# Kernel optimization log

Hardware: AMD Instinct MI355X
Metric: run time of the kernel (lower is better)

Reference implementation:

```python
import jax, jax.numpy as jnp
import numpy as np

N_NODES = 100000
N_EDGES = 1250000
D_FEAT = 64


def setup_inputs() -> dict:
    key = jax.random.key(0)
    kx, ke = jax.random.split(key)
    x = jax.random.normal(kx, (N_NODES, D_FEAT), dtype=jnp.float32)
    edge_index = jax.random.randint(ke, (2, N_EDGES), 0, N_NODES, dtype=jnp.int64)
    return {"x": x, "edge_index": edge_index}


def _aggregate(x, src, dst, num_nodes):
    # out[i] = sum_{e: dst[e]==i} x[src[e]]  (identity message, 'add' aggr)
    return jax.ops.segment_sum(x[src], dst, num_segments=num_nodes)


def reference(x, edge_index):
    num_nodes = x.shape[0]
    src, dst = edge_index[0], edge_index[1]  # PyG source_to_target flow
    h = _aggregate(x, src, dst, num_nodes)   # conv1
    h = jax.nn.relu(h)
    h = _aggregate(h, src, dst, num_nodes)   # conv2
    return h
```

## Files before the change

### kernel.cpp

```cpp
#include <hip/hip_runtime.h>
#include <hip/hip_bf16.h>


#define N_FEAT    64
#define BIN_SHIFT 7
#define BIN_NODES 128
#define CAPBIN    2048
#define NB_H      784
#define NSCAN     1024
#define GSTRIDE   16
#define TILE      4096
#define PTHREADS  512
#define EPT       8
#define NPTR      (BIN_NODES + 1)
#define SRCSH     14

typedef unsigned int u32;
typedef unsigned short u16;
typedef __attribute__((ext_vector_type(8))) unsigned short u16x8;
typedef __attribute__((ext_vector_type(4))) unsigned int u32x4;
typedef __attribute__((ext_vector_type(2))) float f32x2;

__device__ inline u16 f2bf(float f) {
    u32 u = __builtin_bit_cast(u32, f);
    return (u16)((u + 0x7FFFu + ((u >> 16) & 1u)) >> 16);
}

__global__ __launch_bounds__(256) void convert_kernel(
    const float* __restrict__ xf, u16* __restrict__ xb, int n_elems)
{
    int i = ((int)blockIdx.x * 256 + (int)threadIdx.x) * 8;
    if (i < n_elems) {
        float4 a = *(const float4*)(xf + i);
        float4 b = *(const float4*)(xf + i + 4);
        u16x8 r;
        r[0]=f2bf(a.x); r[1]=f2bf(a.y); r[2]=f2bf(a.z); r[3]=f2bf(a.w);
        r[4]=f2bf(b.x); r[5]=f2bf(b.y); r[6]=f2bf(b.z); r[7]=f2bf(b.w);
        *(u16x8*)(xb + i) = r;
    }
}

__global__ __launch_bounds__(PTHREADS) void partition_kernel(
    const int* __restrict__ src, const int* __restrict__ dst,
    u32* __restrict__ gcur,
    u32* __restrict__ cbdata,
    int n_edges, int n_bins)
{
    __shared__ u32 hist[NSCAN];
    __shared__ u32 starts[NSCAN];
    __shared__ u32 lpos[NSCAN];
    __shared__ u32 wcur[NB_H];
    __shared__ u32 sortbuf[TILE];
    __shared__ u16 binid[TILE];
    __shared__ u32 wsum[PTHREADS / 64];

    const int tid   = threadIdx.x;
    const int tbase = (int)blockIdx.x * TILE;
    const int tend  = min(tbase + TILE, n_edges);

    for (int i = tid; i < NSCAN; i += PTHREADS) { hist[i] = 0; lpos[i] = 0; }
    __syncthreads();

    u32 breg[EPT];
    u32 preg[EPT];
    #pragma unroll
    for (int k = 0; k < EPT; ++k) {
        int e = tbase + tid + k * PTHREADS;
        breg[k] = ~0u;
        if (e < tend) {
            int d = dst[e];
            int s = src[e];
            breg[k] = (u32)d >> BIN_SHIFT;
            preg[k] = ((u32)(d & (BIN_NODES - 1)) << 17) | (u32)s;
            atomicAdd(&hist[breg[k]], 1u);
        }
    }
    __syncthreads();

    {
        const int b0 = tid * 2;
        u32 h0 = hist[b0], h1 = hist[b0 + 1];
        u32 s  = h0 + h1;
        u32 inc = s;
        #pragma unroll
        for (int d = 1; d < 64; d <<= 1) {
            u32 o = __shfl_up(inc, d);
            if ((tid & 63) >= d) inc += o;
        }
        if ((tid & 63) == 63) wsum[tid >> 6] = inc;
        __syncthreads();
        u32 woff = 0;
        #pragma unroll
        for (int k = 0; k < PTHREADS / 64; ++k) if (k < (tid >> 6)) woff += wsum[k];
        u32 excl = woff + inc - s;
        starts[b0]     = excl;
        starts[b0 + 1] = excl + h0;
    }
    __syncthreads();

    const int rot = (int)(((u32)blockIdx.x * 193u) % (u32)n_bins);
    for (int i = tid; i < n_bins; i += PTHREADS) {
        int b = i + rot; if (b >= n_bins) b -= n_bins;
        u32 h = hist[b];
        if (h) wcur[b] = atomicAdd(&gcur[b * GSTRIDE], h);
    }
    __syncthreads();

    #pragma unroll
    for (int k = 0; k < EPT; ++k) {
        if (breg[k] != ~0u) {
            u32 b   = breg[k];
            u32 pos = starts[b] + atomicAdd(&lpos[b], 1u);
            sortbuf[pos] = preg[k];
            binid[pos]   = (u16)b;
        }
    }
    __syncthreads();

    const int cnt = tend - tbase;
    for (int j = tid; j < cnt; j += PTHREADS) {
        u32 b   = binid[j];
        u32 rel = wcur[b] + ((u32)j - starts[b]);
        if (rel < CAPBIN)
            cbdata[(size_t)b * CAPBIN + rel] = sortbuf[j];
    }
}

__global__ __launch_bounds__(256) void sort_aggregate_kernel(
    const u16* __restrict__ xin,
    u32* __restrict__ cbdata,
    const u32* __restrict__ gcur,
    u32* __restrict__ nodeptr,
    u16* __restrict__ out_bf,
    int n_nodes, int n_bins)
{
    __shared__ u32 hist[NSCAN];
    __shared__ u32 starts[NSCAN];
    __shared__ u32 lpos[NSCAN];
    __shared__ u32 sl[CAPBIN];
    __shared__ u32 wsum[4];

    const int tid = threadIdx.x;
    const int bin = blockIdx.x;
    if (bin >= n_bins) return;

    for (int i = tid; i < NSCAN; i += 256) { hist[i] = 0; lpos[i] = 0; }
    __syncthreads();

    int cnt = (int)gcur[bin * GSTRIDE];
    if (cnt > CAPBIN) cnt = CAPBIN;
    u32* bd = cbdata + (size_t)bin * CAPBIN;

    for (int j = tid; j < cnt; j += 256) {
        u32 p = bd[j];
        u32 key = ((p >> 17) << 3) | ((p & 0x1FFFFu) >> SRCSH);
        atomicAdd(&hist[key], 1u);
    }
    __syncthreads();

    {
        const int b0 = tid * 4;
        u32 h0 = hist[b0], h1 = hist[b0+1], h2 = hist[b0+2], h3 = hist[b0+3];
        u32 s  = h0 + h1 + h2 + h3;
        u32 inc = s;
        #pragma unroll
        for (int d = 1; d < 64; d <<= 1) {
            u32 o = __shfl_up(inc, d);
            if ((tid & 63) >= d) inc += o;
        }
        if ((tid & 63) == 63) wsum[tid >> 6] = inc;
        __syncthreads();
        u32 woff = 0;
        #pragma unroll
        for (int k = 0; k < 4; ++k) if (k < (tid >> 6)) woff += wsum[k];
        u32 excl = woff + inc - s;
        starts[b0]   = excl;
        starts[b0+1] = excl + h0;
        starts[b0+2] = excl + h0 + h1;
        starts[b0+3] = excl + h0 + h1 + h2;
    }
    __syncthreads();

    for (int j = tid; j < cnt; j += 256) {
        u32 p   = bd[j];
        u32 key = ((p >> 17) << 3) | ((p & 0x1FFFFu) >> SRCSH);
        u32 pos = starts[key] + atomicAdd(&lpos[key], 1u);
        sl[pos] = p & 0x1FFFFu;
    }
    __syncthreads();

    const u32 base = (u32)bin * CAPBIN;
    for (int j = tid; j < cnt; j += 256)
        bd[j] = sl[j];
    if (tid < BIN_NODES)
        nodeptr[(size_t)bin * NPTR + tid] = base + starts[tid << 3];
    if (tid == 0)
        nodeptr[(size_t)bin * NPTR + BIN_NODES] = base + (u32)cnt;

    const int w    = tid >> 6;
    const int lane = tid & 63;
    const int grp  = lane >> 3;
    const int sub  = lane & 7;
    const char* xc = (const char*)xin;

    #pragma unroll 1
    for (int rep = 0; rep < 4; ++rep) {
        const int nid  = w * 8 + grp + rep * 32;
        const int node = bin * BIN_NODES + nid;
        const int s0 = (int)starts[nid << 3];
        const int s1 = (nid < BIN_NODES - 1) ? (int)starts[(nid + 1) << 3] : cnt;

        f32x2 a0={0.f,0.f}, a1={0.f,0.f}, a2={0.f,0.f}, a3={0.f,0.f};

        int jb = s0;
        for (; jb + 8 <= s1; jb += 8) {
            #pragma unroll
            for (int k = 0; k < 8; ++k) {
                u32 s = sl[jb + k];
                u32x4 v = *(const u32x4*)(xc + ((size_t)s << 7) + (sub << 4));
                a0 += (f32x2){ __builtin_bit_cast(float, v[0] << 16),
                               __builtin_bit_cast(float, v[0] & 0xFFFF0000u) };
                a1 += (f32x2){ __builtin_bit_cast(float, v[1] << 16),
                               __builtin_bit_cast(float, v[1] & 0xFFFF0000u) };
                a2 += (f32x2){ __builtin_bit_cast(float, v[2] << 16),
                               __builtin_bit_cast(float, v[2] & 0xFFFF0000u) };
                a3 += (f32x2){ __builtin_bit_cast(float, v[3] << 16),
                               __builtin_bit_cast(float, v[3] & 0xFFFF0000u) };
            }
        }
        #pragma unroll 1
        for (; jb < s1; ++jb) {
            u32 s = sl[jb];
            u32x4 v = *(const u32x4*)(xc + ((size_t)s << 7) + (sub << 4));
            a0 += (f32x2){ __builtin_bit_cast(float, v[0] << 16),
                           __builtin_bit_cast(float, v[0] & 0xFFFF0000u) };
            a1 += (f32x2){ __builtin_bit_cast(float, v[1] << 16),
                           __builtin_bit_cast(float, v[1] & 0xFFFF0000u) };
            a2 += (f32x2){ __builtin_bit_cast(float, v[2] << 16),
                           __builtin_bit_cast(float, v[2] & 0xFFFF0000u) };
            a3 += (f32x2){ __builtin_bit_cast(float, v[3] << 16),
                           __builtin_bit_cast(float, v[3] & 0xFFFF0000u) };
        }

        if (node < n_nodes) {
            u16x8 o;
            o[0]=f2bf(fmaxf(a0.x,0.f)); o[1]=f2bf(fmaxf(a0.y,0.f));
            o[2]=f2bf(fmaxf(a1.x,0.f)); o[3]=f2bf(fmaxf(a1.y,0.f));
            o[4]=f2bf(fmaxf(a2.x,0.f)); o[5]=f2bf(fmaxf(a2.y,0.f));
            o[6]=f2bf(fmaxf(a3.x,0.f)); o[7]=f2bf(fmaxf(a3.y,0.f));
            *(u16x8*)(out_bf + (size_t)node * N_FEAT + sub * 8) = o;
        }
    }
}

__global__ __launch_bounds__(256) void aggregate_kernel(
    const u16* __restrict__ xin,
    const u32* __restrict__ csorted,
    const u32* __restrict__ nodeptr,
    float* __restrict__ out_f,
    int n_nodes)
{
    const int tid  = threadIdx.x;

    const int w    = tid >> 6;
    const int lane = tid & 63;
    const int grp  = lane >> 3;
    const int sub  = lane & 7;
    const char* xc = (const char*)xin;

    const int nl   = w * 8 + grp;
    const int node = (int)blockIdx.x * 32 + nl;
    const int bin  = node >> BIN_SHIFT;
    const int nid  = node & (BIN_NODES - 1);

    const int s0  = (int)nodeptr[(size_t)bin * NPTR + nid];
    const int s1  = (int)nodeptr[(size_t)bin * NPTR + nid + 1];

    f32x2 a0={0.f,0.f}, a1={0.f,0.f}, a2={0.f,0.f}, a3={0.f,0.f};

    int jb = s0;
    for (; jb + 8 <= s1; jb += 8) {
        u32 myid = csorted[jb + sub];
        #pragma unroll
        for (int k = 0; k < 8; ++k) {
            u32 s = (u32)__shfl((int)myid, (lane & 56) + k, 64);
            u32x4 v = *(const u32x4*)(xc + ((size_t)s << 7) + (sub << 4));
            a0 += (f32x2){ __builtin_bit_cast(float, v[0] << 16),
                           __builtin_bit_cast(float, v[0] & 0xFFFF0000u) };
            a1 += (f32x2){ __builtin_bit_cast(float, v[1] << 16),
                           __builtin_bit_cast(float, v[1] & 0xFFFF0000u) };
            a2 += (f32x2){ __builtin_bit_cast(float, v[2] << 16),
                           __builtin_bit_cast(float, v[2] & 0xFFFF0000u) };
            a3 += (f32x2){ __builtin_bit_cast(float, v[3] << 16),
                           __builtin_bit_cast(float, v[3] & 0xFFFF0000u) };
        }
    }
    if (jb < s1) {
        u32 myid = 0;
        if (jb + sub < s1) myid = csorted[jb + sub];
        const int m = s1 - jb;
        #pragma unroll 1
        for (int k = 0; k < m; ++k) {
            u32 s = (u32)__shfl((int)myid, (lane & 56) + k, 64);
            u32x4 v = *(const u32x4*)(xc + ((size_t)s << 7) + (sub << 4));
            a0 += (f32x2){ __builtin_bit_cast(float, v[0] << 16),
                           __builtin_bit_cast(float, v[0] & 0xFFFF0000u) };
            a1 += (f32x2){ __builtin_bit_cast(float, v[1] << 16),
                           __builtin_bit_cast(float, v[1] & 0xFFFF0000u) };
            a2 += (f32x2){ __builtin_bit_cast(float, v[2] << 16),
                           __builtin_bit_cast(float, v[2] & 0xFFFF0000u) };
            a3 += (f32x2){ __builtin_bit_cast(float, v[3] << 16),
                           __builtin_bit_cast(float, v[3] & 0xFFFF0000u) };
        }
    }

    if (node < n_nodes) {
        float* dp = out_f + (size_t)node * N_FEAT + sub * 8;
        *(float4*)dp       = (float4){a0.x, a0.y, a1.x, a1.y};
        *(float4*)(dp + 4) = (float4){a2.x, a2.y, a3.x, a3.y};
    }
}

extern "C" void kernel_launch(void* const* d_in, const int* in_sizes, int n_in,
                              void* d_out, int out_size, void* d_ws, size_t ws_size,
                              hipStream_t stream) {
    const float* x          = (const float*)d_in[0];
    const int*   edge_index = (const int*)d_in[1];

    const int n_edges = in_sizes[1] / 2;
    const int* src = edge_index;
    const int* dst = edge_index + n_edges;

    const int n_nodes = out_size / N_FEAT;
    const int n_bins  = (n_nodes + BIN_NODES - 1) >> BIN_SHIFT;
    float* out = (float*)d_out;

    const size_t xb_bytes    = (size_t)out_size * sizeof(u16);
    const size_t hb_bytes    = (size_t)out_size * sizeof(u16);
    const size_t cb_bytes    = (size_t)n_bins * CAPBIN * sizeof(u32);
    const size_t np_bytes    = (size_t)n_bins * NPTR * sizeof(u32);
    const size_t gcur_bytes  = (size_t)NB_H * GSTRIDE * sizeof(u32);

    char* w = (char*)d_ws;
    u16* xb      = (u16*)w;              w += xb_bytes;
    u16* hb      = (u16*)w;              w += hb_bytes;
    u32* cbdata  = (u32*)w;              w += cb_bytes;
    u32* nodeptr = (u32*)w;              w += np_bytes;
    u32* gcur    = (u32*)w;

    hipMemsetAsync(gcur, 0, gcur_bytes, stream);

    const int conv_blocks = (out_size / 8 + 255) / 256;
    convert_kernel<<<conv_blocks, 256, 0, stream>>>(x, xb, out_size);

    const int part_blocks = (n_edges + TILE - 1) / TILE;
    partition_kernel<<<part_blocks, PTHREADS, 0, stream>>>(
        src, dst, gcur, cbdata, n_edges, n_bins);

    sort_aggregate_kernel<<<n_bins, 256, 0, stream>>>(
        xb, cbdata, gcur, nodeptr, hb, n_nodes, n_bins);

    const int agg_blocks = (n_nodes + 31) / 32;
    aggregate_kernel<<<agg_blocks, 256, 0, stream>>>(hb, cbdata, nodeptr, out, n_nodes);
}
```

Baseline: 162.1 us.

## Replace global-atomic bin scatter with per-tile sorted runs gathered per bin

The partition kernel no longer reserves space in each bin with global atomics and scatters edges into per-bin buckets. Instead it writes each tile's bin-sorted edges contiguously and stores the per-tile bin start offsets as u16. The sort/aggregate kernel then gathers its bin's segment from every tile into shared memory before sorting. This drops the memset, the global atomic traffic and the scattered writes. In exchange each bin block does many small, uncoalesced per-tile reads with a serial copy loop per thread.

New measurement: 153.7 us. 1.05x faster.

```diff
diff --git a/kernel.cpp b/kernel.cpp
--- a/kernel.cpp
+++ b/kernel.cpp
@@ -6,13 +6,12 @@
 #define BIN_SHIFT 7
 #define BIN_NODES 128
 #define CAPBIN    2048
-#define NB_H      784
 #define NSCAN     1024
-#define GSTRIDE   16
 #define TILE      4096
 #define PTHREADS  512
 #define EPT       8
 #define NPTR      (BIN_NODES + 1)
+#define TSP       784
 #define SRCSH     14
 
 typedef unsigned int u32;
@@ -42,20 +41,19 @@
 
 __global__ __launch_bounds__(PTHREADS) void partition_kernel(
     const int* __restrict__ src, const int* __restrict__ dst,
-    u32* __restrict__ gcur,
-    u32* __restrict__ cbdata,
-    int n_edges, int n_bins)
+    u32* __restrict__ ebdata,
+    u16* __restrict__ ts16,
+    int n_edges)
 {
     __shared__ u32 hist[NSCAN];
     __shared__ u32 starts[NSCAN];
     __shared__ u32 lpos[NSCAN];
-    __shared__ u32 wcur[NB_H];
     __shared__ u32 sortbuf[TILE];
-    __shared__ u16 binid[TILE];
     __shared__ u32 wsum[PTHREADS / 64];
 
     const int tid   = threadIdx.x;
-    const int tbase = (int)blockIdx.x * TILE;
+    const int tile  = (int)blockIdx.x;
+    const int tbase = tile * TILE;
     const int tend  = min(tbase + TILE, n_edges);
 
     for (int i = tid; i < NSCAN; i += PTHREADS) { hist[i] = 0; lpos[i] = 0; }
@@ -98,61 +96,68 @@
     }
     __syncthreads();
 
-    const int rot = (int)(((u32)blockIdx.x * 193u) % (u32)n_bins);
-    for (int i = tid; i < n_bins; i += PTHREADS) {
-        int b = i + rot; if (b >= n_bins) b -= n_bins;
-        u32 h = hist[b];
-        if (h) wcur[b] = atomicAdd(&gcur[b * GSTRIDE], h);
-    }
-    __syncthreads();
-
     #pragma unroll
     for (int k = 0; k < EPT; ++k) {
         if (breg[k] != ~0u) {
             u32 b   = breg[k];
             u32 pos = starts[b] + atomicAdd(&lpos[b], 1u);
             sortbuf[pos] = preg[k];
-            binid[pos]   = (u16)b;
         }
     }
     __syncthreads();
 
     const int cnt = tend - tbase;
-    for (int j = tid; j < cnt; j += PTHREADS) {
-        u32 b   = binid[j];
-        u32 rel = wcur[b] + ((u32)j - starts[b]);
-        if (rel < CAPBIN)
-            cbdata[(size_t)b * CAPBIN + rel] = sortbuf[j];
-    }
+    for (int j = tid; j < cnt; j += PTHREADS)
+        ebdata[(size_t)tbase + j] = sortbuf[j];
+    for (int i = tid; i < TSP; i += PTHREADS)
+        ts16[(size_t)tile * TSP + i] = (u16)starts[i];
 }
 
 __global__ __launch_bounds__(256) void sort_aggregate_kernel(
     const u16* __restrict__ xin,
+    const u32* __restrict__ ebdata,
+    const u16* __restrict__ ts16,
     u32* __restrict__ cbdata,
-    const u32* __restrict__ gcur,
     u32* __restrict__ nodeptr,
     u16* __restrict__ out_bf,
-    int n_nodes, int n_bins)
+    int n_nodes, int n_bins, int n_tiles)
 {
     __shared__ u32 hist[NSCAN];
     __shared__ u32 starts[NSCAN];
     __shared__ u32 lpos[NSCAN];
+    __shared__ u32 ebuf[CAPBIN];
     __shared__ u32 sl[CAPBIN];
     __shared__ u32 wsum[4];
+    __shared__ u32 ecnt;
 
     const int tid = threadIdx.x;
     const int bin = blockIdx.x;
     if (bin >= n_bins) return;
 
     for (int i = tid; i < NSCAN; i += 256) { hist[i] = 0; lpos[i] = 0; }
-    __syncthreads();
-
-    int cnt = (int)gcur[bin * GSTRIDE];
+    if (tid == 0) ecnt = 0;
+    __syncthreads();
+
+    for (int t = tid; t < n_tiles; t += 256) {
+        u32 s0 = (u32)ts16[(size_t)t * TSP + bin];
+        u32 s1 = (u32)ts16[(size_t)t * TSP + bin + 1];
+        int len = (int)(s1 - s0);
+        if (len > 0) {
+            u32 base = atomicAdd(&ecnt, (u32)len);
+            const u32* sp = ebdata + (size_t)t * TILE + s0;
+            for (int i = 0; i < len; ++i) {
+                u32 pos = base + (u32)i;
+                if (pos < CAPBIN) ebuf[pos] = sp[i];
+            }
+        }
+    }
+    __syncthreads();
+
+    int cnt = (int)ecnt;
     if (cnt > CAPBIN) cnt = CAPBIN;
-    u32* bd = cbdata + (size_t)bin * CAPBIN;
 
     for (int j = tid; j < cnt; j += 256) {
-        u32 p = bd[j];
+        u32 p = ebuf[j];
         u32 key = ((p >> 17) << 3) | ((p & 0x1FFFFu) >> SRCSH);
         atomicAdd(&hist[key], 1u);
     }
@@ -182,7 +187,7 @@
     __syncthreads();
 
     for (int j = tid; j < cnt; j += 256) {
-        u32 p   = bd[j];
+        u32 p   = ebuf[j];
         u32 key = ((p >> 17) << 3) | ((p & 0x1FFFFu) >> SRCSH);
         u32 pos = starts[key] + atomicAdd(&lpos[key], 1u);
         sl[pos] = p & 0x1FFFFu;
@@ -191,7 +196,7 @@
 
     const u32 base = (u32)bin * CAPBIN;
     for (int j = tid; j < cnt; j += 256)
-        bd[j] = sl[j];
+        cbdata[(size_t)base + j] = sl[j];
     if (tid < BIN_NODES)
         nodeptr[(size_t)bin * NPTR + tid] = base + starts[tid << 3];
     if (tid == 0)
@@ -333,32 +338,32 @@
 
     const int n_nodes = out_size / N_FEAT;
     const int n_bins  = (n_nodes + BIN_NODES - 1) >> BIN_SHIFT;
+    const int n_tiles = (n_edges + TILE - 1) / TILE;
     float* out = (float*)d_out;
 
-    const size_t xb_bytes    = (size_t)out_size * sizeof(u16);
-    const size_t hb_bytes    = (size_t)out_size * sizeof(u16);
-    const size_t cb_bytes    = (size_t)n_bins * CAPBIN * sizeof(u32);
-    const size_t np_bytes    = (size_t)n_bins * NPTR * sizeof(u32);
-    const size_t gcur_bytes  = (size_t)NB_H * GSTRIDE * sizeof(u32);
+    const size_t xb_bytes = (size_t)out_size * sizeof(u16);
+    const size_t hb_bytes = (size_t)out_size * sizeof(u16);
+    const size_t eb_bytes = (size_t)n_tiles * TILE * sizeof(u32);
+    const size_t cb_bytes = (size_t)n_bins * CAPBIN * sizeof(u32);
+    const size_t ts_bytes = (size_t)n_tiles * TSP * sizeof(u16);
+    const size_t np_bytes = (size_t)n_bins * NPTR * sizeof(u32);
 
     char* w = (char*)d_ws;
     u16* xb      = (u16*)w;              w += xb_bytes;
     u16* hb      = (u16*)w;              w += hb_bytes;
+    u32* ebdata  = (u32*)w;              w += eb_bytes;
     u32* cbdata  = (u32*)w;              w += cb_bytes;
+    u16* ts16    = (u16*)w;              w += ts_bytes;
     u32* nodeptr = (u32*)w;              w += np_bytes;
-    u32* gcur    = (u32*)w;
-
-    hipMemsetAsync(gcur, 0, gcur_bytes, stream);
 
     const int conv_blocks = (out_size / 8 + 255) / 256;
     convert_kernel<<<conv_blocks, 256, 0, stream>>>(x, xb, out_size);
 
-    const int part_blocks = (n_edges + TILE - 1) / TILE;
-    partition_kernel<<<part_blocks, PTHREADS, 0, stream>>>(
-        src, dst, gcur, cbdata, n_edges, n_bins);
+    partition_kernel<<<n_tiles, PTHREADS, 0, stream>>>(
+        src, dst, ebdata, ts16, n_edges);
 
     sort_aggregate_kernel<<<n_bins, 256, 0, stream>>>(
-        xb, cbdata, gcur, nodeptr, hb, n_nodes, n_bins);
+        xb, ebdata, ts16, cbdata, nodeptr, hb, n_nodes, n_bins, n_tiles);
 
     const int agg_blocks = (n_nodes + 31) / 32;
     aggregate_kernel<<<agg_blocks, 256, 0, stream>>>(hb, cbdata, nodeptr, out, n_nodes);
```
